# Kernel tuning notes

Hardware: AMD Instinct MI355X
Metric: run time of the kernel (lower is better)

The kernel has to match this reference:

```python
import jax, jax.numpy as jnp
import numpy as np

N = 16384          # num nodes (adj is dense NxN)
INPUT_DIM = 512
HIDDEN = 128
E_POS = 524288
E_NEG = 524288


def setup_inputs() -> dict:
    key = jax.random.key(0)
    k1, k2, k3, k4, k5, k6, k7 = jax.random.split(key, 7)
    X = jax.random.normal(k1, (N, INPUT_DIM), dtype=jnp.float32)
    adj = jax.random.uniform(k2, (N, N), dtype=jnp.float32)
    train_edges = jax.random.randint(k3, (E_POS, 2), 0, N, dtype=jnp.int64)
    train_false_edges = jax.random.randint(k4, (E_NEG, 2), 0, N, dtype=jnp.int64)
    # parameters (xavier / kaiming scale approximated with uniform bounds)
    b1 = float(np.sqrt(6.0 / (INPUT_DIM + HIDDEN)))
    weight = jax.random.uniform(k5, (INPUT_DIM, HIDDEN), minval=-b1, maxval=b1, dtype=jnp.float32)
    b2 = float(np.sqrt(6.0 / (2 * HIDDEN + HIDDEN)))
    weight_two = jax.random.uniform(k6, (2 * HIDDEN, HIDDEN), minval=-b2, maxval=b2, dtype=jnp.float32)
    b3 = float(np.sqrt(6.0 / HIDDEN) / np.sqrt(2.0))  # kaiming_uniform a=1
    weight_three = jax.random.uniform(k7, (HIDDEN, 1), minval=-b3, maxval=b3, dtype=jnp.float32)
    return {"X": X, "adj": adj, "weight": weight, "weight_two": weight_two,
            "weight_three": weight_three, "train_edges": train_edges,
            "train_false_edges": train_false_edges}


def reference(X, adj, weight, weight_two, weight_three, train_edges, train_false_edges):
    # encode: Z = adj @ (X @ W)
    Z = adj @ (X @ weight)                                  # [N, H]
    edges = jnp.concatenate([train_edges, train_false_edges], axis=0)  # [E, 2]
    # decode: vectorized gather-concat replacing the per-edge Python loop
    z_pair = jnp.concatenate([Z[edges[:, 0]], Z[edges[:, 1]]], axis=1)  # [E, 2H]
    h = jax.nn.relu(z_pair) @ weight_two @ weight_three      # [E, 1]
    return jax.nn.sigmoid(h)
```

## Files before the change

### kernel.cpp

```cpp
#include <hip/hip_runtime.h>


#define N_NODES 16384
#define IN_DIM  512
#define HID     128
#define E_POS_N 524288
#define E_TOT   1048576

typedef __bf16 bf16x8 __attribute__((ext_vector_type(8)));
typedef float  f32x4  __attribute__((ext_vector_type(4)));
typedef unsigned short us8 __attribute__((ext_vector_type(8)));
typedef unsigned short us4 __attribute__((ext_vector_type(4)));

__device__ __forceinline__ bf16x8 ldsb(const void* p){
  return __builtin_bit_cast(bf16x8, *reinterpret_cast<const us8*>(p));
}
__device__ __forceinline__ void gload16(const void* g, void* l){
  __builtin_amdgcn_global_load_lds(
      (const __attribute__((address_space(1))) unsigned int*)g,
      (__attribute__((address_space(3))) unsigned int*)l, 16, 0, 0);
}

__device__ __forceinline__ void split8(const float* f, bf16x8& hi, bf16x8& lo){
  unsigned u[8];
#pragma unroll
  for (int i = 0; i < 8; ++i) u[i] = __float_as_uint(f[i]);
  uint4 hv;
  hv.x = __builtin_amdgcn_perm(u[1], u[0], 0x07060302u);
  hv.y = __builtin_amdgcn_perm(u[3], u[2], 0x07060302u);
  hv.z = __builtin_amdgcn_perm(u[5], u[4], 0x07060302u);
  hv.w = __builtin_amdgcn_perm(u[7], u[6], 0x07060302u);
  hi = __builtin_bit_cast(bf16x8, hv);
  bf16x8 lv;
#pragma unroll
  for (int i = 0; i < 8; ++i)
    lv[i] = (__bf16)(f[i] - __uint_as_float(u[i] & 0xFFFF0000u));
  lo = lv;
}

__global__ __launch_bounds__(512) void prep_kernel(const float* __restrict__ W,
                                                   const float* __restrict__ w2,
                                                   const float* __restrict__ w3,
                                                   unsigned short* __restrict__ bfW,
                                                   float* __restrict__ w23){
  const int blk = blockIdx.x, tid = threadIdx.x;
  if (blk < 16){
    const int c = tid & 127, g = tid >> 7;
    float f[8];
#pragma unroll
    for (int j = 0; j < 8; ++j) f[j] = W[(blk * 32 + g * 8 + j) * HID + c];
    bf16x8 hi, lo; split8(f, hi, lo);
    const int sw = (c & 7) << 4;
    char* tb = (char*)bfW + blk * 16384 + c * 128;
    *(us8*)(tb + ((g * 16) ^ sw))      = __builtin_bit_cast(us8, hi);
    *(us8*)(tb + ((64 + g * 16) ^ sw)) = __builtin_bit_cast(us8, lo);
  } else if (tid < 256){
    float acc = 0.f;
#pragma unroll 4
    for (int k = 0; k < HID; ++k) acc = fmaf(w2[tid * HID + k], w3[k], acc);
    w23[tid] = acc;
  }
}

__global__ __launch_bounds__(256) void xw_kernel(const float* __restrict__ X,
                                                 const unsigned short* __restrict__ bfW,
                                                 unsigned short* __restrict__ bfB){
  __shared__ alignas(16) char lds[4][24576];
  const int tid = threadIdx.x, lane = tid & 63, w = tid >> 6;
  const int blk = blockIdx.x;
  const int g = lane >> 4, l15 = lane & 15;

  int aoff[4][2], boffH[2], boffL[2];
#pragma unroll
  for (int m = 0; m < 4; ++m){
    const int r = m * 16 + l15, sw = (r & 7) << 4;
    aoff[m][0] = r * 128 + ((g * 32) ^ sw);
    aoff[m][1] = r * 128 + ((g * 32 + 16) ^ sw);
  }
#pragma unroll
  for (int n = 0; n < 2; ++n){
    const int c = (w & 3) * 32 + n * 16 + l15, sw = (c & 7) << 4;
    boffH[n] = 8192 + c * 128 + ((g * 16) ^ sw);
    boffL[n] = 8192 + c * 128 + ((64 + g * 16) ^ sw);
  }

  const char* xsrc[2];
#pragma unroll
  for (int i = 0; i < 2; ++i){
    const int r = i * 32 + (tid >> 3);
    xsrc[i] = (const char*)X + ((size_t)(blk * 64 + r) * IN_DIM) * 4
            + (((tid & 7) * 16) ^ ((r & 7) << 4));
  }
  const char* bsrc = (const char*)bfW + tid * 16;

#define XSTAGE(buf, tt) do { \
    gload16(xsrc[0] + (tt) * 128, (buf) + tid * 16); \
    gload16(xsrc[1] + (tt) * 128, (buf) + 4096 + tid * 16); \
    gload16(bsrc + (size_t)(tt) * 16384,         (buf) + 8192  + tid * 16); \
    gload16(bsrc + (size_t)(tt) * 16384 + 4096,  (buf) + 12288 + tid * 16); \
    gload16(bsrc + (size_t)(tt) * 16384 + 8192,  (buf) + 16384 + tid * 16); \
    gload16(bsrc + (size_t)(tt) * 16384 + 12288, (buf) + 20480 + tid * 16); \
  } while (0)

  f32x4 acc[4][2] = {};
  auto compute = [&](const char* bp){
    bf16x8 bHv[2], bLv[2];
#pragma unroll
    for (int n = 0; n < 2; ++n){ bHv[n] = ldsb(bp + boffH[n]); bLv[n] = ldsb(bp + boffL[n]); }
#pragma unroll
    for (int m = 0; m < 4; ++m){
      f32x4 v0 = *(const f32x4*)(bp + aoff[m][0]);
      f32x4 v1 = *(const f32x4*)(bp + aoff[m][1]);
      float f[8] = {v0[0], v0[1], v0[2], v0[3], v1[0], v1[1], v1[2], v1[3]};
      bf16x8 aH, aL; split8(f, aH, aL);
      __builtin_amdgcn_s_setprio(1);
#pragma unroll
      for (int n = 0; n < 2; ++n) acc[m][n] = __builtin_amdgcn_mfma_f32_16x16x32_bf16(aH, bHv[n], acc[m][n], 0, 0, 0);
#pragma unroll
      for (int n = 0; n < 2; ++n) acc[m][n] = __builtin_amdgcn_mfma_f32_16x16x32_bf16(aH, bLv[n], acc[m][n], 0, 0, 0);
#pragma unroll
      for (int n = 0; n < 2; ++n) acc[m][n] = __builtin_amdgcn_mfma_f32_16x16x32_bf16(aL, bHv[n], acc[m][n], 0, 0, 0);
      __builtin_amdgcn_s_setprio(0);
    }
  };

  XSTAGE(lds[0], 0); XSTAGE(lds[1], 1); XSTAGE(lds[2], 2);
  asm volatile("s_waitcnt vmcnt(12)" ::: "memory");
  __builtin_amdgcn_s_barrier();

  const int nt = IN_DIM / 32;
#pragma unroll 1
  for (int t = 0; t < nt; ++t){
    char* bp = lds[t & 3];
    if (t + 3 < nt) XSTAGE(lds[(t + 3) & 3], t + 3);
    compute(bp);
    if (t + 3 < nt)      asm volatile("s_waitcnt vmcnt(12)" ::: "memory");
    else if (t + 2 < nt) asm volatile("s_waitcnt vmcnt(6)" ::: "memory");
    else if (t + 1 < nt) asm volatile("s_waitcnt vmcnt(0)" ::: "memory");
    if (t + 1 < nt) __builtin_amdgcn_s_barrier();
  }
#undef XSTAGE

#pragma unroll
  for (int m = 0; m < 4; ++m){
#pragma unroll
    for (int n = 0; n < 2; ++n){
      const int col = (w & 3) * 32 + n * 16 + l15;
      const int T   = 2 * blk + (m >> 1);
      const int g2  = (2 * m + (g >> 1)) & 3;
      const int sw  = (col & 7) << 4;
      char* tb = (char*)bfB + (size_t)T * 16384 + col * 128;
      uint2 hv;
      hv.x = __builtin_amdgcn_perm(__float_as_uint(acc[m][n][1]), __float_as_uint(acc[m][n][0]), 0x07060302u);
      hv.y = __builtin_amdgcn_perm(__float_as_uint(acc[m][n][3]), __float_as_uint(acc[m][n][2]), 0x07060302u);
      us4 lv;
#pragma unroll
      for (int j = 0; j < 4; ++j){
        unsigned u = __float_as_uint(acc[m][n][j]);
        lv[j] = __builtin_bit_cast(unsigned short,
                 (__bf16)(acc[m][n][j] - __uint_as_float(u & 0xFFFF0000u)));
      }
      *(uint2*)(tb + (((g2 * 16) ^ sw) + (g & 1) * 8))      = hv;
      *(uint2*)(tb + (((64 + g2 * 16) ^ sw) + (g & 1) * 8)) = __builtin_bit_cast(uint2, lv);
    }
  }
}

__global__ __launch_bounds__(512, 2) void zgemm_kernel(const float* __restrict__ adj,
                                                       const unsigned short* __restrict__ bfB,
                                                       float* __restrict__ part){
  __shared__ alignas(16) char lds[4][32768];
  const int tid = threadIdx.x, lane = tid & 63, w = tid >> 6;
  const int wm = w >> 2, wn = w & 3;
  const int xcd = blockIdx.x & 7;
  const int s   = xcd & 1;
  const int mt  = (xcd >> 1) * 32 + (blockIdx.x >> 3);
  const int k0  = s * (N_NODES / 2);
  const int nt  = (N_NODES / 2) / 32;
  const int g = lane >> 4, l15 = lane & 15;

  int aoff[4][2], boffH[2], boffL[2];
#pragma unroll
  for (int m = 0; m < 4; ++m){
    const int r = wm * 64 + m * 16 + l15, sw = (r & 7) << 4;
    aoff[m][0] = r * 128 + ((g * 32) ^ sw);
    aoff[m][1] = r * 128 + ((g * 32 + 16) ^ sw);
  }
#pragma unroll
  for (int n = 0; n < 2; ++n){
    const int c = wn * 32 + n * 16 + l15, sw = (c & 7) << 4;
    boffH[n] = 16384 + c * 128 + ((g * 16) ^ sw);
    boffL[n] = 16384 + c * 128 + ((64 + g * 16) ^ sw);
  }

  const char* asrc[2];
#pragma unroll
  for (int i = 0; i < 2; ++i){
    const int r = i * 64 + (tid >> 3);
    asrc[i] = (const char*)adj + ((size_t)(mt * 128 + r) * N_NODES + k0) * 4
            + (((tid & 7) * 16) ^ ((r & 7) << 4));
  }
  const char* bsrc = (const char*)bfB + (size_t)(k0 >> 5) * 16384 + tid * 16;

#define ZSTAGE(buf, tt) do { \
    gload16(asrc[0] + (size_t)(tt) * 128, (buf) + tid * 16); \
    gload16(asrc[1] + (size_t)(tt) * 128, (buf) + 8192 + tid * 16); \
    gload16(bsrc + (size_t)(tt) * 16384,        (buf) + 16384 + tid * 16); \
    gload16(bsrc + (size_t)(tt) * 16384 + 8192, (buf) + 24576 + tid * 16); \
  } while (0)

  f32x4 acc[4][2] = {};
  auto compute = [&](const char* bp){
    bf16x8 bHv[2], bLv[2];
#pragma unroll
    for (int n = 0; n < 2; ++n){ bHv[n] = ldsb(bp + boffH[n]); bLv[n] = ldsb(bp + boffL[n]); }
#pragma unroll
    for (int m = 0; m < 4; ++m){
      f32x4 v0 = *(const f32x4*)(bp + aoff[m][0]);
      f32x4 v1 = *(const f32x4*)(bp + aoff[m][1]);
      float f[8] = {v0[0], v0[1], v0[2], v0[3], v1[0], v1[1], v1[2], v1[3]};
      bf16x8 aH, aL; split8(f, aH, aL);
      __builtin_amdgcn_s_setprio(1);
#pragma unroll
      for (int n = 0; n < 2; ++n) acc[m][n] = __builtin_amdgcn_mfma_f32_16x16x32_bf16(aH, bHv[n], acc[m][n], 0, 0, 0);
#pragma unroll
      for (int n = 0; n < 2; ++n) acc[m][n] = __builtin_amdgcn_mfma_f32_16x16x32_bf16(aH, bLv[n], acc[m][n], 0, 0, 0);
#pragma unroll
      for (int n = 0; n < 2; ++n) acc[m][n] = __builtin_amdgcn_mfma_f32_16x16x32_bf16(aL, bHv[n], acc[m][n], 0, 0, 0);
      __builtin_amdgcn_s_setprio(0);
    }
  };

  ZSTAGE(lds[0], 0); ZSTAGE(lds[1], 1); ZSTAGE(lds[2], 2);
  asm volatile("s_waitcnt vmcnt(8)" ::: "memory");
  __builtin_amdgcn_s_barrier();

#pragma unroll 1
  for (int t = 0; t < nt; ++t){
    char* bp = lds[t & 3];
    if (t + 3 < nt) ZSTAGE(lds[(t + 3) & 3], t + 3);
    compute(bp);
    if (t + 3 < nt)      asm volatile("s_waitcnt vmcnt(8)" ::: "memory");
    else if (t + 2 < nt) asm volatile("s_waitcnt vmcnt(4)" ::: "memory");
    else if (t + 1 < nt) asm volatile("s_waitcnt vmcnt(0)" ::: "memory");
    if (t + 1 < nt) __builtin_amdgcn_s_barrier();
  }
#undef ZSTAGE

  float* pb = part + (size_t)s * ((size_t)N_NODES * HID);
  const int row0 = mt * 128 + wm * 64;
  const int col0 = wn * 32;
#pragma unroll
  for (int m = 0; m < 4; ++m){
#pragma unroll
    for (int n = 0; n < 2; ++n){
#pragma unroll
      for (int j = 0; j < 4; ++j){
        const int row = row0 + m * 16 + g * 4 + j;
        const int col = col0 + n * 16 + l15;
        pb[(size_t)row * HID + col] = acc[m][n][j];
      }
    }
  }
}

__global__ __launch_bounds__(256) void nodered_kernel(const float* __restrict__ part,
                                                      const float* __restrict__ w23,
                                                      float* __restrict__ aarr,
                                                      float* __restrict__ barr){
  const int lane = threadIdx.x & 63, wv = threadIdx.x >> 6;
  const int n0 = blockIdx.x * 16 + wv * 4;
  const float w1a = w23[lane],       w1b = w23[lane + 64];
  const float w2a = w23[128 + lane], w2b = w23[192 + lane];
  const float* p0 = part + (size_t)n0 * HID;
  const float* p1 = p0 + (size_t)N_NODES * HID;
  float av[4], bv[4];
#pragma unroll
  for (int u = 0; u < 4; ++u){
    float z1 = p0[u * HID + lane]      + p1[u * HID + lane];
    float z2 = p0[u * HID + lane + 64] + p1[u * HID + lane + 64];
    z1 = fmaxf(z1, 0.f); z2 = fmaxf(z2, 0.f);
    av[u] = z1 * w1a + z2 * w1b;
    bv[u] = z1 * w2a + z2 * w2b;
  }
#pragma unroll
  for (int u = 0; u < 4; ++u){
#pragma unroll
    for (int o = 32; o > 0; o >>= 1){
      av[u] += __shfl_down(av[u], o);
      bv[u] += __shfl_down(bv[u], o);
    }
  }
  if (lane == 0){
#pragma unroll
    for (int u = 0; u < 4; ++u){ aarr[n0 + u] = av[u]; barr[n0 + u] = bv[u]; }
  }
}

__global__ __launch_bounds__(256) void edge_kernel(const int* __restrict__ e0,
                                                   const int* __restrict__ e1,
                                                   const float* __restrict__ aarr,
                                                   const float* __restrict__ barr,
                                                   float* __restrict__ out){
  const int e = (blockIdx.x * 256 + threadIdx.x) * 4;
  const int* ep; int eb;
  if (e < E_POS_N){ ep = e0; eb = e; } else { ep = e1; eb = e - E_POS_N; }
  int4 p0 = *(const int4*)(ep + 2 * eb);
  int4 p1 = *(const int4*)(ep + 2 * eb + 4);
  float4 o;
  o.x = aarr[p0.x] + barr[p0.y];
  o.y = aarr[p0.z] + barr[p0.w];
  o.z = aarr[p1.x] + barr[p1.y];
  o.w = aarr[p1.z] + barr[p1.w];
  o.x = 1.f / (1.f + __expf(-o.x));
  o.y = 1.f / (1.f + __expf(-o.y));
  o.z = 1.f / (1.f + __expf(-o.z));
  o.w = 1.f / (1.f + __expf(-o.w));
  *(float4*)(out + e) = o;
}

extern "C" void kernel_launch(void* const* d_in, const int* in_sizes, int n_in,
                              void* d_out, int out_size, void* d_ws, size_t ws_size,
                              hipStream_t stream){
  const float* X   = (const float*)d_in[0];
  const float* adj = (const float*)d_in[1];
  const float* W   = (const float*)d_in[2];
  const float* W2  = (const float*)d_in[3];
  const float* W3  = (const float*)d_in[4];
  const int*   e0  = (const int*)d_in[5];
  const int*   e1  = (const int*)d_in[6];
  float* out = (float*)d_out;

  char* wsb = (char*)d_ws;
  const size_t MB = 1024 * 1024;
  unsigned short* bfB = (unsigned short*)(wsb);
  unsigned short* bfW = (unsigned short*)(wsb + 8 * MB);
  float* w23  = (float*)(wsb + 8 * MB + 512 * 1024);
  float* aarr = (float*)(wsb + 9 * MB);
  float* barr = (float*)(wsb + 9 * MB + 64 * 1024);
  float* part = (float*)(wsb + 16 * MB);

  hipLaunchKernelGGL(prep_kernel, dim3(17), dim3(512), 0, stream, W, W2, W3, bfW, w23);
  hipLaunchKernelGGL(xw_kernel, dim3(N_NODES / 64), dim3(256), 0, stream, X, bfW, bfB);
  hipLaunchKernelGGL(zgemm_kernel, dim3(256), dim3(512), 0, stream, adj, bfB, part);
  hipLaunchKernelGGL(nodered_kernel, dim3(N_NODES / 16), dim3(256), 0, stream,
                     part, w23, aarr, barr);
  hipLaunchKernelGGL(edge_kernel, dim3(E_TOT / 1024), dim3(256), 0, stream,
                     e0, e1, aarr, barr, out);
}
```

Measured before the change: 330.3 us.

## Split adj GEMM K into four slices, double-buffer LDS, and reshape the wave tiling

The Z = adj·(XW) GEMM now splits the K dimension four ways instead of two and launches 512 blocks instead of 256. LDS staging shrinks from a 4-deep to a 2-deep buffer with barrier-guarded refills, which allows four blocks per CU for occupancy. Wave tiling changes from 4x2 to 2x4 subtiles, so each A split is reused over more B columns. The cost is twice as many fp32 partial sums to write and reduce in nodered, plus a shallower prefetch pipeline.

```diff
diff --git a/kernel.cpp b/kernel.cpp
--- a/kernel.cpp
+++ b/kernel.cpp
@@ -166,29 +166,29 @@
   }
 }
 
-__global__ __launch_bounds__(512, 2) void zgemm_kernel(const float* __restrict__ adj,
+__global__ __launch_bounds__(512, 4) void zgemm_kernel(const float* __restrict__ adj,
                                                        const unsigned short* __restrict__ bfB,
                                                        float* __restrict__ part){
-  __shared__ alignas(16) char lds[4][32768];
+  __shared__ alignas(16) char lds[2][32768];
   const int tid = threadIdx.x, lane = tid & 63, w = tid >> 6;
-  const int wm = w >> 2, wn = w & 3;
+  const int wm = w >> 1, wn = w & 1;
   const int xcd = blockIdx.x & 7;
-  const int s   = xcd & 1;
-  const int mt  = (xcd >> 1) * 32 + (blockIdx.x >> 3);
-  const int k0  = s * (N_NODES / 2);
-  const int nt  = (N_NODES / 2) / 32;
+  const int s   = xcd & 3;
+  const int mt  = ((xcd >> 2) << 6) + (blockIdx.x >> 3);
+  const int k0  = s * (N_NODES / 4);
+  const int nt  = (N_NODES / 4) / 32;
   const int g = lane >> 4, l15 = lane & 15;
 
-  int aoff[4][2], boffH[2], boffL[2];
-#pragma unroll
-  for (int m = 0; m < 4; ++m){
-    const int r = wm * 64 + m * 16 + l15, sw = (r & 7) << 4;
+  int aoff[2][2], boffH[4], boffL[4];
+#pragma unroll
+  for (int m = 0; m < 2; ++m){
+    const int r = wm * 32 + m * 16 + l15, sw = (r & 7) << 4;
     aoff[m][0] = r * 128 + ((g * 32) ^ sw);
     aoff[m][1] = r * 128 + ((g * 32 + 16) ^ sw);
   }
 #pragma unroll
-  for (int n = 0; n < 2; ++n){
-    const int c = wn * 32 + n * 16 + l15, sw = (c & 7) << 4;
+  for (int n = 0; n < 4; ++n){
+    const int c = wn * 64 + n * 16 + l15, sw = (c & 7) << 4;
     boffH[n] = 16384 + c * 128 + ((g * 16) ^ sw);
     boffL[n] = 16384 + c * 128 + ((64 + g * 16) ^ sw);
   }
@@ -209,51 +209,55 @@
     gload16(bsrc + (size_t)(tt) * 16384 + 8192, (buf) + 24576 + tid * 16); \
   } while (0)
 
-  f32x4 acc[4][2] = {};
+  f32x4 acc[2][4] = {};
   auto compute = [&](const char* bp){
-    bf16x8 bHv[2], bLv[2];
-#pragma unroll
-    for (int n = 0; n < 2; ++n){ bHv[n] = ldsb(bp + boffH[n]); bLv[n] = ldsb(bp + boffL[n]); }
-#pragma unroll
-    for (int m = 0; m < 4; ++m){
+    bf16x8 bHv[4], bLv[4];
+#pragma unroll
+    for (int n = 0; n < 4; ++n){ bHv[n] = ldsb(bp + boffH[n]); bLv[n] = ldsb(bp + boffL[n]); }
+#pragma unroll
+    for (int m = 0; m < 2; ++m){
       f32x4 v0 = *(const f32x4*)(bp + aoff[m][0]);
       f32x4 v1 = *(const f32x4*)(bp + aoff[m][1]);
       float f[8] = {v0[0], v0[1], v0[2], v0[3], v1[0], v1[1], v1[2], v1[3]};
       bf16x8 aH, aL; split8(f, aH, aL);
       __builtin_amdgcn_s_setprio(1);
 #pragma unroll
-      for (int n = 0; n < 2; ++n) acc[m][n] = __builtin_amdgcn_mfma_f32_16x16x32_bf16(aH, bHv[n], acc[m][n], 0, 0, 0);
-#pragma unroll
-      for (int n = 0; n < 2; ++n) acc[m][n] = __builtin_amdgcn_mfma_f32_16x16x32_bf16(aH, bLv[n], acc[m][n], 0, 0, 0);
-#pragma unroll
-      for (int n = 0; n < 2; ++n) acc[m][n] = __builtin_amdgcn_mfma_f32_16x16x32_bf16(aL, bHv[n], acc[m][n], 0, 0, 0);
+      for (int n = 0; n < 4; ++n) acc[m][n] = __builtin_amdgcn_mfma_f32_16x16x32_bf16(aH, bHv[n], acc[m][n], 0, 0, 0);
+#pragma unroll
+      for (int n = 0; n < 4; ++n) acc[m][n] = __builtin_amdgcn_mfma_f32_16x16x32_bf16(aH, bLv[n], acc[m][n], 0, 0, 0);
+#pragma unroll
+      for (int n = 0; n < 4; ++n) acc[m][n] = __builtin_amdgcn_mfma_f32_16x16x32_bf16(aL, bHv[n], acc[m][n], 0, 0, 0);
       __builtin_amdgcn_s_setprio(0);
     }
   };
 
-  ZSTAGE(lds[0], 0); ZSTAGE(lds[1], 1); ZSTAGE(lds[2], 2);
-  asm volatile("s_waitcnt vmcnt(8)" ::: "memory");
+  ZSTAGE(lds[0], 0); ZSTAGE(lds[1], 1);
+  asm volatile("s_waitcnt vmcnt(4)" ::: "memory");
   __builtin_amdgcn_s_barrier();
+  __builtin_amdgcn_sched_barrier(0);
 
 #pragma unroll 1
   for (int t = 0; t < nt; ++t){
-    char* bp = lds[t & 3];
-    if (t + 3 < nt) ZSTAGE(lds[(t + 3) & 3], t + 3);
-    compute(bp);
-    if (t + 3 < nt)      asm volatile("s_waitcnt vmcnt(8)" ::: "memory");
-    else if (t + 2 < nt) asm volatile("s_waitcnt vmcnt(4)" ::: "memory");
-    else if (t + 1 < nt) asm volatile("s_waitcnt vmcnt(0)" ::: "memory");
-    if (t + 1 < nt) __builtin_amdgcn_s_barrier();
+    compute(lds[t & 1]);
+    __builtin_amdgcn_sched_barrier(0);
+    __builtin_amdgcn_s_barrier();
+    if (t + 2 < nt) ZSTAGE(lds[t & 1], t + 2);
+    if (t + 1 < nt){
+      if (t + 2 < nt) asm volatile("s_waitcnt vmcnt(4)" ::: "memory");
+      else            asm volatile("s_waitcnt vmcnt(0)" ::: "memory");
+      __builtin_amdgcn_s_barrier();
+      __builtin_amdgcn_sched_barrier(0);
+    }
   }
 #undef ZSTAGE
 
   float* pb = part + (size_t)s * ((size_t)N_NODES * HID);
-  const int row0 = mt * 128 + wm * 64;
-  const int col0 = wn * 32;
-#pragma unroll
-  for (int m = 0; m < 4; ++m){
-#pragma unroll
-    for (int n = 0; n < 2; ++n){
+  const int row0 = mt * 128 + wm * 32;
+  const int col0 = wn * 64;
+#pragma unroll
+  for (int m = 0; m < 2; ++m){
+#pragma unroll
+    for (int n = 0; n < 4; ++n){
 #pragma unroll
       for (int j = 0; j < 4; ++j){
         const int row = row0 + m * 16 + g * 4 + j;
@@ -272,13 +276,17 @@
   const int n0 = blockIdx.x * 16 + wv * 4;
   const float w1a = w23[lane],       w1b = w23[lane + 64];
   const float w2a = w23[128 + lane], w2b = w23[192 + lane];
-  const float* p0 = part + (size_t)n0 * HID;
-  const float* p1 = p0 + (size_t)N_NODES * HID;
+  const float* p = part + (size_t)n0 * HID;
+  const size_t NH = (size_t)N_NODES * HID;
   float av[4], bv[4];
 #pragma unroll
   for (int u = 0; u < 4; ++u){
-    float z1 = p0[u * HID + lane]      + p1[u * HID + lane];
-    float z2 = p0[u * HID + lane + 64] + p1[u * HID + lane + 64];
+    float z1 = 0.f, z2 = 0.f;
+#pragma unroll
+    for (int sI = 0; sI < 4; ++sI){
+      z1 += p[sI * NH + u * HID + lane];
+      z2 += p[sI * NH + u * HID + lane + 64];
+    }
     z1 = fmaxf(z1, 0.f); z2 = fmaxf(z2, 0.f);
     av[u] = z1 * w1a + z2 * w1b;
     bv[u] = z1 * w2a + z2 * w2b;
@@ -342,7 +350,7 @@
 
   hipLaunchKernelGGL(prep_kernel, dim3(17), dim3(512), 0, stream, W, W2, W3, bfW, w23);
   hipLaunchKernelGGL(xw_kernel, dim3(N_NODES / 64), dim3(256), 0, stream, X, bfW, bfB);
-  hipLaunchKernelGGL(zgemm_kernel, dim3(256), dim3(512), 0, stream, adj, bfB, part);
+  hipLaunchKernelGGL(zgemm_kernel, dim3(512), dim3(512), 0, stream, adj, bfB, part);
   hipLaunchKernelGGL(nodered_kernel, dim3(N_NODES / 16), dim3(256), 0, stream,
                      part, w23, aarr, barr);
   hipLaunchKernelGGL(edge_kernel, dim3(E_TOT / 1024), dim3(256), 0, stream,
```

Result: faster. 294.7 us (-10.8%).
